# Kernel optimization log

Hardware: AMD Instinct MI355X
Metric: run time of the kernel (lower is better)

The kernel has to match this reference:

```python
import jax, jax.numpy as jnp
import numpy as np

NUM_CLASSES = 81
THRESHOLD = 0.5
NEGPOS_RATIO = 3
VAR0, VAR1 = 0.1, 0.2
B, P, T = 64, 25000, 16


def setup_inputs() -> dict:
    key = jax.random.key(0)
    k1, k2, k3, k4, k5, k6 = jax.random.split(key, 6)
    loc_data = jax.random.normal(k1, (B, P, 4), dtype=jnp.float32)
    conf_data = jax.random.normal(k2, (B, P, NUM_CLASSES), dtype=jnp.float32)
    # priors in center-offset form (cx, cy, w, h), all in (0,1), w/h > 0
    centers = jax.random.uniform(k3, (P, 2), minval=0.05, maxval=0.95)
    wh = jax.random.uniform(k4, (P, 2), minval=0.05, maxval=0.3)
    priors = jnp.concatenate([centers, wh], axis=1).astype(jnp.float32)
    # ground-truth boxes in corner form (xmin, ymin, xmax, ymax), valid (max > min)
    pts = jax.random.uniform(k5, (B, T, 2, 2), minval=0.0, maxval=0.98)
    mn = jnp.min(pts, axis=2)
    mx = jnp.max(pts, axis=2) + 0.02  # strictly positive width/height
    boxes = jnp.concatenate([mn, jnp.clip(mx, 0.0, 1.0)], axis=-1)
    labels = jax.random.randint(k6, (B, T), 0, NUM_CLASSES - 1).astype(jnp.float32)
    targets = jnp.concatenate([boxes, labels[..., None]], axis=-1)
    return {"loc_data": loc_data, "conf_data": conf_data, "priors": priors, "targets": targets}


def point_form(p):
    # (cx,cy,w,h) -> (xmin,ymin,xmax,ymax)
    return jnp.concatenate([p[:, :2] - p[:, 2:] / 2, p[:, :2] + p[:, 2:] / 2], axis=1)


def jaccard(a, b):
    # a: [T,4], b: [P,4], corner form -> IoU [T,P]
    lt = jnp.maximum(a[:, None, :2], b[None, :, :2])
    rb = jnp.minimum(a[:, None, 2:], b[None, :, 2:])
    wh = jnp.clip(rb - lt, 0.0)
    inter = wh[..., 0] * wh[..., 1]
    area_a = ((a[:, 2] - a[:, 0]) * (a[:, 3] - a[:, 1]))[:, None]
    area_b = ((b[:, 2] - b[:, 0]) * (b[:, 3] - b[:, 1]))[None, :]
    return inter / (area_a + area_b - inter)


def encode(matched, priors):
    # SSD offset encoding with variances
    g_cxcy = ((matched[:, :2] + matched[:, 2:]) * 0.5 - priors[:, :2]) / (VAR0 * priors[:, 2:])
    g_wh = jnp.log((matched[:, 2:] - matched[:, :2]) / priors[:, 2:]) / VAR1
    return jnp.concatenate([g_cxcy, g_wh], axis=1)


def match_one(truths, labels, priors):
    # truths: [T,4] corner, labels: [T], priors: [P,4] center
    overlaps = jaccard(truths, point_form(priors))        # [T,P]
    best_prior_idx = jnp.argmax(overlaps, axis=1)         # [T]
    best_truth_overlap = jnp.max(overlaps, axis=0)        # [P]
    best_truth_idx = jnp.argmax(overlaps, axis=0)         # [P]
    best_truth_overlap = best_truth_overlap.at[best_prior_idx].set(2.0)
    for j in range(T):
        best_truth_idx = best_truth_idx.at[best_prior_idx[j]].set(j)
    matched = truths[best_truth_idx]                      # [P,4]
    conf = labels[best_truth_idx].astype(jnp.int32) + 1
    conf = jnp.where(best_truth_overlap < THRESHOLD, 0, conf)
    return encode(matched, priors), conf


def smooth_l1(d):
    ad = jnp.abs(d)
    return jnp.where(ad < 1.0, 0.5 * d * d, ad - 0.5)


def reference(loc_data, conf_data, priors, targets):
    truths = jax.lax.stop_gradient(targets[..., :4])  # .data in torch
    labels = jax.lax.stop_gradient(targets[..., 4])
    loc_t, conf_t = jax.vmap(match_one, in_axes=(0, 0, None))(truths, labels, priors)
    pos = conf_t > 0                                      # [B,P]
    num_priors = pos.shape[1]
    # localization: smooth-L1 summed over positive priors (masked instead of boolean gather)
    loss_l = jnp.sum(jnp.where(pos[..., None], smooth_l1(loc_data - loc_t), 0.0))
    # per-prior conf loss = logsumexp - logit[target]
    lse = jax.nn.logsumexp(conf_data, axis=-1)            # [B,P]
    conf_gt = jnp.take_along_axis(conf_data, conf_t[..., None], axis=-1)[..., 0]
    ce = lse - conf_gt
    # hard negative mining: zero positives, double argsort rank
    loss_c = jnp.where(pos, 0.0, ce)
    loss_idx = jnp.argsort(-loss_c, axis=1)
    idx_rank = jnp.argsort(loss_idx, axis=1)
    num_pos = jnp.sum(pos, axis=1, keepdims=True)
    num_neg = jnp.minimum(NEGPOS_RATIO * num_pos, num_priors - 1)
    neg = idx_rank < num_neg
    # cross-entropy summed over positives + mined negatives
    loss_conf = jnp.sum(jnp.where(pos | neg, ce, 0.0))
    N = jnp.maximum(jnp.sum(num_pos).astype(loc_data.dtype), 1.0)
    return loss_l / N, loss_conf / N
```

## Files before the change

### kernel.cpp

```cpp
#include <hip/hip_runtime.h>

namespace {

constexpr int kB = 64;
constexpr int kP = 25000;
constexpr int kT = 16;
constexpr int kC = 81;
constexpr int kRowsPerBlk = 64;
constexpr int kChunks = 16;
constexpr int kChunkP = (kP + kChunks - 1) / kChunks;
constexpr float kThresh = 0.5f;

__device__ __forceinline__ float smooth_l1(float d) {
  float ad = fabsf(d);
  return ad < 1.0f ? 0.5f * d * d : ad - 0.5f;
}

__global__ __launch_bounds__(256) void match1_kernel(
    const float* __restrict__ priors,
    const float* __restrict__ targets,
    unsigned char* __restrict__ mcode,
    unsigned long long* __restrict__ best_prior) {
  const int chunk = blockIdx.x;
  const int b = blockIdx.y;
  const int tid = threadIdx.x;
  const int p0 = chunk * kChunkP;
  const int p1 = min(p0 + kChunkP, kP);

  __shared__ float tx0[kT], ty0[kT], tx1[kT], ty1[kT], tarea[kT];
  __shared__ float swv[kT][4];
  __shared__ int swi[kT][4];

  if (tid < kT) {
    const float* tg = targets + (b * kT + tid) * 5;
    float x0 = tg[0], y0 = tg[1], x1 = tg[2], y1 = tg[3];
    tx0[tid] = x0; ty0[tid] = y0; tx1[tid] = x1; ty1[tid] = y1;
    tarea[tid] = (x1 - x0) * (y1 - y0);
  }
  __syncthreads();

  float bestv[kT];
  int besti[kT];
#pragma unroll
  for (int t = 0; t < kT; ++t) { bestv[t] = -1.0f; besti[t] = 0; }

  for (int p = p0 + tid; p < p1; p += 256) {
    float4 pr = reinterpret_cast<const float4*>(priors)[p];
    float px0 = pr.x - pr.z * 0.5f, py0 = pr.y - pr.w * 0.5f;
    float px1 = pr.x + pr.z * 0.5f, py1 = pr.y + pr.w * 0.5f;
    float parea = (px1 - px0) * (py1 - py0);
    float mv = -1.0f;
    int mt = 0;
#pragma unroll
    for (int t = 0; t < kT; ++t) {
      float lx = fmaxf(tx0[t], px0), ly = fmaxf(ty0[t], py0);
      float rx = fminf(tx1[t], px1), ry = fminf(ty1[t], py1);
      float w = fmaxf(rx - lx, 0.0f), h = fmaxf(ry - ly, 0.0f);
      float inter = w * h;
      float iou = inter / (tarea[t] + parea - inter);
      if (iou > bestv[t]) { bestv[t] = iou; besti[t] = p; }
      if (iou > mv) { mv = iou; mt = t; }
    }
    mcode[b * kP + p] = (unsigned char)(mt | (mv < kThresh ? 0x80 : 0));
  }

#pragma unroll
  for (int t = 0; t < kT; ++t) {
    float v = bestv[t];
    int i = besti[t];
    for (int off = 32; off > 0; off >>= 1) {
      float v2 = __shfl_xor(v, off, 64);
      int i2 = __shfl_xor(i, off, 64);
      if (v2 > v || (v2 == v && i2 < i)) { v = v2; i = i2; }
    }
    if ((tid & 63) == 0) { swv[t][tid >> 6] = v; swi[t][tid >> 6] = i; }
  }
  __syncthreads();
  if (tid < kT) {
    float v = swv[tid][0];
    int i = swi[tid][0];
#pragma unroll
    for (int w = 1; w < 4; ++w) {
      float v2 = swv[tid][w];
      int i2 = swi[tid][w];
      if (v2 > v || (v2 == v && i2 < i)) { v = v2; i = i2; }
    }
    unsigned long long pk = ((unsigned long long)__float_as_uint(v) << 32) |
                            (unsigned long long)(0xFFFFFFFFu - (unsigned)i);
    atomicMax(&best_prior[b * kT + tid], pk);
  }
}

__global__ __launch_bounds__(256) void match2_kernel(
    const float* __restrict__ loc_data,
    const float* __restrict__ priors,
    const float* __restrict__ targets,
    const unsigned long long* __restrict__ best_prior,
    unsigned char* __restrict__ code,
    int* __restrict__ num_pos,
    float* __restrict__ loss_l_acc) {
  const int chunk = blockIdx.x;
  const int b = blockIdx.y;
  const int tid = threadIdx.x;
  const int p0 = chunk * kChunkP;
  const int p1 = min(p0 + kChunkP, kP);

  __shared__ int s_bp[kT];
  __shared__ float sx0[kT], sy0[kT], sx1[kT], sy1[kT], slab[kT];
  __shared__ float swf[4];
  __shared__ int swi[4];

  if (tid < kT) {
    s_bp[tid] = (int)(0xFFFFFFFFu -
                      (unsigned)(best_prior[b * kT + tid] & 0xFFFFFFFFull));
    const float* tg = targets + (b * kT + tid) * 5;
    sx0[tid] = tg[0]; sy0[tid] = tg[1]; sx1[tid] = tg[2]; sy1[tid] = tg[3];
    slab[tid] = tg[4];
  }
  __syncthreads();

  float lsum = 0.0f;
  int pcount = 0;
  for (int p = p0 + tid; p < p1; p += 256) {
    int c = code[b * kP + p];
    int mt = c & 0x0F;
    bool neg = (c & 0x80) != 0;
    bool forced = false;
#pragma unroll
    for (int j = 0; j < kT; ++j) {
      if (s_bp[j] == p) { mt = j; forced = true; }
    }
    int conf = (!forced && neg) ? 0 : ((int)slab[mt] + 1);
    code[b * kP + p] = (unsigned char)conf;
    if (conf > 0) {
      ++pcount;
      float4 pr = reinterpret_cast<const float4*>(priors)[p];
      float mx0 = sx0[mt], my0 = sy0[mt], mx1 = sx1[mt], my1 = sy1[mt];
      float gcx = ((mx0 + mx1) * 0.5f - pr.x) / (0.1f * pr.z);
      float gcy = ((my0 + my1) * 0.5f - pr.y) / (0.1f * pr.w);
      float gw = logf((mx1 - mx0) / pr.z) / 0.2f;
      float gh = logf((my1 - my0) / pr.w) / 0.2f;
      float4 ld = reinterpret_cast<const float4*>(loc_data)[b * kP + p];
      lsum += smooth_l1(ld.x - gcx) + smooth_l1(ld.y - gcy) +
              smooth_l1(ld.z - gw) + smooth_l1(ld.w - gh);
    }
  }
  for (int off = 32; off > 0; off >>= 1) {
    lsum += __shfl_down(lsum, off, 64);
    pcount += __shfl_down(pcount, off, 64);
  }
  if ((tid & 63) == 0) { swf[tid >> 6] = lsum; swi[tid >> 6] = pcount; }
  __syncthreads();
  if (tid == 0) {
    float lt = swf[0] + swf[1] + swf[2] + swf[3];
    int pt = swi[0] + swi[1] + swi[2] + swi[3];
    if (lt != 0.0f) atomicAdd(loss_l_acc, lt);
    if (pt != 0) atomicAdd(&num_pos[b], pt);
  }
}

__global__ __launch_bounds__(256) void ce_kernel(
    const float* __restrict__ conf_data,
    const unsigned char* __restrict__ conf_t,
    float* __restrict__ loss_c,
    float* __restrict__ pos_ce_acc) {
  __shared__ float tile[kRowsPerBlk * kC];
  __shared__ float swsum[4];
  const int tid = threadIdx.x;
  const long long base = (long long)blockIdx.x * (kRowsPerBlk * kC);
  const float4* src = reinterpret_cast<const float4*>(conf_data + base);
  float4* dst = reinterpret_cast<float4*>(tile);
#pragma unroll
  for (int i = 0; i < 6; ++i) {
    int idx = tid + i * 256;
    if (idx < kRowsPerBlk * kC / 4) dst[idx] = src[idx];
  }
  __syncthreads();

  const int r = tid >> 2;
  const int sub = tid & 3;
  const float* x = tile + r * kC;
  float m = -3.0e38f;
  for (int j = sub; j < kC; j += 4) m = fmaxf(m, x[j]);
  m = fmaxf(m, __shfl_xor(m, 1, 64));
  m = fmaxf(m, __shfl_xor(m, 2, 64));
  float s = 0.0f;
  for (int j = sub; j < kC; j += 4) s += __expf(x[j] - m);
  s += __shfl_xor(s, 1, 64);
  s += __shfl_xor(s, 2, 64);
  float posce = 0.0f;
  if (sub == 0) {
    const long long row = (long long)blockIdx.x * kRowsPerBlk + r;
    float lse = __logf(s) + m;
    int ct = conf_t[row];
    float ce = lse - x[ct];
    bool pos = ct > 0;
    loss_c[row] = pos ? 0.0f : ce;
    posce = pos ? ce : 0.0f;
  }
  for (int off = 32; off > 0; off >>= 1) posce += __shfl_down(posce, off, 64);
  if ((tid & 63) == 0) swsum[tid >> 6] = posce;
  __syncthreads();
  if (tid == 0) {
    float t = swsum[0] + swsum[1] + swsum[2] + swsum[3];
    if (t != 0.0f) atomicAdd(pos_ce_acc, t);
  }
}

__global__ __launch_bounds__(256) void select_kernel(
    const float* __restrict__ loss_c,
    const int* __restrict__ num_pos,
    float* __restrict__ acc,
    int* __restrict__ counter,
    float* __restrict__ out) {
  const int b = blockIdx.x;
  const int tid = threadIdx.x;
  const int k = min(3 * num_pos[b], kP - 1);
  __shared__ int swi[4];
  __shared__ float swf[4];

  if (k > 0) {
    constexpr int kV4 = kP / 4;
    constexpr int kPer = (kV4 + 255) / 256;
    const float4* v4 = reinterpret_cast<const float4*>(loss_c + (long long)b * kP);
    float4 lv[kPer];
#pragma unroll
    for (int j = 0; j < kPer; ++j) {
      int i = tid + j * 256;
      lv[j] = (i < kV4) ? v4[i] : float4{0.0f, 0.0f, 0.0f, 0.0f};
    }

    unsigned int ans = 0;
    for (int bit = 30; bit >= 0; --bit) {
      const unsigned int cand = ans | (1u << bit);
      int cnt = 0;
#pragma unroll
      for (int j = 0; j < kPer; ++j) {
        cnt += (__float_as_uint(lv[j].x) >= cand) + (__float_as_uint(lv[j].y) >= cand) +
               (__float_as_uint(lv[j].z) >= cand) + (__float_as_uint(lv[j].w) >= cand);
      }
      for (int off = 32; off > 0; off >>= 1) cnt += __shfl_down(cnt, off, 64);
      if ((tid & 63) == 0) swi[tid >> 6] = cnt;
      __syncthreads();
      int tot = swi[0] + swi[1] + swi[2] + swi[3];
      if (tot >= k) ans = cand;
      __syncthreads();
    }
    float sum = 0.0f;
    int cgt = 0;
#pragma unroll
    for (int j = 0; j < kPer; ++j) {
      if (__float_as_uint(lv[j].x) > ans) { sum += lv[j].x; ++cgt; }
      if (__float_as_uint(lv[j].y) > ans) { sum += lv[j].y; ++cgt; }
      if (__float_as_uint(lv[j].z) > ans) { sum += lv[j].z; ++cgt; }
      if (__float_as_uint(lv[j].w) > ans) { sum += lv[j].w; ++cgt; }
    }
    for (int off = 32; off > 0; off >>= 1) {
      sum += __shfl_down(sum, off, 64);
      cgt += __shfl_down(cgt, off, 64);
    }
    if ((tid & 63) == 0) { swf[tid >> 6] = sum; swi[tid >> 6] = cgt; }
    __syncthreads();
    if (tid == 0) {
      float st = swf[0] + swf[1] + swf[2] + swf[3];
      int ct = swi[0] + swi[1] + swi[2] + swi[3];
      atomicAdd(acc + 2, st + (float)(k - ct) * __uint_as_float(ans));
    }
  }

  __threadfence();
  if (tid == 0) {
    int done = atomicAdd(counter, 1);
    if (done == kB - 1) {
      int np = 0;
      for (int i = 0; i < kB; ++i) np += num_pos[i];
      float N = fmaxf((float)np, 1.0f);
      float neg = atomicAdd(acc + 2, 0.0f);
      out[0] = acc[0] / N;
      out[1] = (acc[1] + neg) / N;
    }
  }
}

}

extern "C" void kernel_launch(void* const* d_in, const int* in_sizes, int n_in,
                              void* d_out, int out_size, void* d_ws, size_t ws_size,
                              hipStream_t stream) {
  const float* loc_data = (const float*)d_in[0];
  const float* conf_data = (const float*)d_in[1];
  const float* priors = (const float*)d_in[2];
  const float* targets = (const float*)d_in[3];
  float* out = (float*)d_out;

  char* ws = (char*)d_ws;
  float* loss_c = (float*)ws;
  unsigned char* code = (unsigned char*)(ws + 6400000);
  unsigned long long* best_prior = (unsigned long long*)(ws + 8000000);
  int* num_pos = (int*)(ws + 8008192);
  float* acc = (float*)(ws + 8008448);
  int* counter = (int*)(ws + 8008512);

  hipMemsetAsync(ws + 8000000, 0, 8576, stream);
  hipLaunchKernelGGL(match1_kernel, dim3(kChunks, kB), dim3(256), 0, stream,
                     priors, targets, code, best_prior);
  hipLaunchKernelGGL(match2_kernel, dim3(kChunks, kB), dim3(256), 0, stream,
                     loc_data, priors, targets, best_prior, code, num_pos, acc + 0);
  hipLaunchKernelGGL(ce_kernel, dim3(kB * kP / kRowsPerBlk), dim3(256), 0, stream,
                     conf_data, code, loss_c, acc + 1);
  hipLaunchKernelGGL(select_kernel, dim3(kB), dim3(256), 0, stream,
                     loss_c, num_pos, acc, counter, out);
}
```

Before: 830.3 us.

## Fuse match finalization and localization loss into the cross-entropy kernel

The second matching pass (forced-match resolution, conf target, smooth-L1 localization loss) moves into the per-row cross-entropy kernel, so the code array is no longer rewritten and re-read between kernels. The global atomicMax over best priors becomes per-chunk partial results that the fused kernel reduces on load. The separate memset is dropped by zeroing the accumulators inside the first kernel. This removes one kernel launch, a memset and one pass over the code array, in exchange for redundant best-prior reductions in every CE block and boundary handling for blocks that span two batch items.

```diff
diff --git a/kernel.cpp b/kernel.cpp
--- a/kernel.cpp
+++ b/kernel.cpp
@@ -20,12 +20,21 @@
     const float* __restrict__ priors,
     const float* __restrict__ targets,
     unsigned char* __restrict__ mcode,
-    unsigned long long* __restrict__ best_prior) {
+    unsigned long long* __restrict__ best_pc,
+    int* __restrict__ num_pos,
+    float* __restrict__ acc,
+    int* __restrict__ counter) {
   const int chunk = blockIdx.x;
   const int b = blockIdx.y;
   const int tid = threadIdx.x;
   const int p0 = chunk * kChunkP;
   const int p1 = min(p0 + kChunkP, kP);
+
+  if (chunk == 0 && b == 0) {
+    if (tid < kB) num_pos[tid] = 0;
+    else if (tid < kB + 3) acc[tid - kB] = 0.0f;
+    else if (tid == kB + 3) *counter = 0;
+  }
 
   __shared__ float tx0[kT], ty0[kT], tx1[kT], ty1[kT], tarea[kT];
   __shared__ float swv[kT][4];
@@ -87,93 +96,56 @@
     }
     unsigned long long pk = ((unsigned long long)__float_as_uint(v) << 32) |
                             (unsigned long long)(0xFFFFFFFFu - (unsigned)i);
-    atomicMax(&best_prior[b * kT + tid], pk);
-  }
-}
-
-__global__ __launch_bounds__(256) void match2_kernel(
+    best_pc[((size_t)b * kT + tid) * kChunks + chunk] = pk;
+  }
+}
+
+__global__ __launch_bounds__(256) void ce_fused_kernel(
+    const float* __restrict__ conf_data,
+    const unsigned char* __restrict__ mcode,
     const float* __restrict__ loc_data,
     const float* __restrict__ priors,
     const float* __restrict__ targets,
-    const unsigned long long* __restrict__ best_prior,
-    unsigned char* __restrict__ code,
+    const unsigned long long* __restrict__ best_pc,
+    float* __restrict__ loss_c,
     int* __restrict__ num_pos,
-    float* __restrict__ loss_l_acc) {
-  const int chunk = blockIdx.x;
-  const int b = blockIdx.y;
+    float* __restrict__ acc) {
+  __shared__ float tile[kRowsPerBlk * kC];
+  __shared__ unsigned char smc[kRowsPerBlk];
+  __shared__ int s_bp[2][kT];
+  __shared__ float sx0[2][kT], sy0[2][kT], sx1[2][kT], sy1[2][kT], slab[2][kT];
+  __shared__ float swf_l[4], swf_p[4];
+  __shared__ int swi0[4], swi1[4];
+
   const int tid = threadIdx.x;
-  const int p0 = chunk * kChunkP;
-  const int p1 = min(p0 + kChunkP, kP);
-
-  __shared__ int s_bp[kT];
-  __shared__ float sx0[kT], sy0[kT], sx1[kT], sy1[kT], slab[kT];
-  __shared__ float swf[4];
-  __shared__ int swi[4];
-
-  if (tid < kT) {
-    s_bp[tid] = (int)(0xFFFFFFFFu -
-                      (unsigned)(best_prior[b * kT + tid] & 0xFFFFFFFFull));
-    const float* tg = targets + (b * kT + tid) * 5;
-    sx0[tid] = tg[0]; sy0[tid] = tg[1]; sx1[tid] = tg[2]; sy1[tid] = tg[3];
-    slab[tid] = tg[4];
-  }
-  __syncthreads();
-
-  float lsum = 0.0f;
-  int pcount = 0;
-  for (int p = p0 + tid; p < p1; p += 256) {
-    int c = code[b * kP + p];
-    int mt = c & 0x0F;
-    bool neg = (c & 0x80) != 0;
-    bool forced = false;
-#pragma unroll
-    for (int j = 0; j < kT; ++j) {
-      if (s_bp[j] == p) { mt = j; forced = true; }
-    }
-    int conf = (!forced && neg) ? 0 : ((int)slab[mt] + 1);
-    code[b * kP + p] = (unsigned char)conf;
-    if (conf > 0) {
-      ++pcount;
-      float4 pr = reinterpret_cast<const float4*>(priors)[p];
-      float mx0 = sx0[mt], my0 = sy0[mt], mx1 = sx1[mt], my1 = sy1[mt];
-      float gcx = ((mx0 + mx1) * 0.5f - pr.x) / (0.1f * pr.z);
-      float gcy = ((my0 + my1) * 0.5f - pr.y) / (0.1f * pr.w);
-      float gw = logf((mx1 - mx0) / pr.z) / 0.2f;
-      float gh = logf((my1 - my0) / pr.w) / 0.2f;
-      float4 ld = reinterpret_cast<const float4*>(loc_data)[b * kP + p];
-      lsum += smooth_l1(ld.x - gcx) + smooth_l1(ld.y - gcy) +
-              smooth_l1(ld.z - gw) + smooth_l1(ld.w - gh);
-    }
-  }
-  for (int off = 32; off > 0; off >>= 1) {
-    lsum += __shfl_down(lsum, off, 64);
-    pcount += __shfl_down(pcount, off, 64);
-  }
-  if ((tid & 63) == 0) { swf[tid >> 6] = lsum; swi[tid >> 6] = pcount; }
-  __syncthreads();
-  if (tid == 0) {
-    float lt = swf[0] + swf[1] + swf[2] + swf[3];
-    int pt = swi[0] + swi[1] + swi[2] + swi[3];
-    if (lt != 0.0f) atomicAdd(loss_l_acc, lt);
-    if (pt != 0) atomicAdd(&num_pos[b], pt);
-  }
-}
-
-__global__ __launch_bounds__(256) void ce_kernel(
-    const float* __restrict__ conf_data,
-    const unsigned char* __restrict__ conf_t,
-    float* __restrict__ loss_c,
-    float* __restrict__ pos_ce_acc) {
-  __shared__ float tile[kRowsPerBlk * kC];
-  __shared__ float swsum[4];
-  const int tid = threadIdx.x;
-  const long long base = (long long)blockIdx.x * (kRowsPerBlk * kC);
-  const float4* src = reinterpret_cast<const float4*>(conf_data + base);
+  const long long base = (long long)blockIdx.x * kRowsPerBlk;
+  const int b0 = (int)(base / kP);
+  const long long split = (long long)(b0 + 1) * kP;
+
+  const float4* src = reinterpret_cast<const float4*>(conf_data + base * kC);
   float4* dst = reinterpret_cast<float4*>(tile);
 #pragma unroll
   for (int i = 0; i < 6; ++i) {
     int idx = tid + i * 256;
     if (idx < kRowsPerBlk * kC / 4) dst[idx] = src[idx];
+  }
+  if (tid < kRowsPerBlk / 4)
+    reinterpret_cast<unsigned int*>(smc)[tid] =
+        reinterpret_cast<const unsigned int*>(mcode + base)[tid];
+  if (tid < 2 * kT) {
+    const int which = tid >> 4, t = tid & 15;
+    const int b = b0 + which;
+    if (b < kB) {
+      const unsigned long long* pc = best_pc + ((size_t)b * kT + t) * kChunks;
+      unsigned long long m = pc[0];
+#pragma unroll
+      for (int c = 1; c < kChunks; ++c) { unsigned long long v = pc[c]; m = v > m ? v : m; }
+      s_bp[which][t] = (int)(0xFFFFFFFFu - (unsigned)(m & 0xFFFFFFFFull));
+      const float* tg = targets + ((size_t)b * kT + t) * 5;
+      sx0[which][t] = tg[0]; sy0[which][t] = tg[1];
+      sx1[which][t] = tg[2]; sy1[which][t] = tg[3];
+      slab[which][t] = tg[4];
+    }
   }
   __syncthreads();
 
@@ -188,22 +160,61 @@
   for (int j = sub; j < kC; j += 4) s += __expf(x[j] - m);
   s += __shfl_xor(s, 1, 64);
   s += __shfl_xor(s, 2, 64);
-  float posce = 0.0f;
+
+  float lsum = 0.0f, posce = 0.0f;
+  int pc0 = 0, pc1 = 0;
   if (sub == 0) {
-    const long long row = (long long)blockIdx.x * kRowsPerBlk + r;
+    const long long row = base + r;
+    const int which = (row >= split) ? 1 : 0;
+    const int p = (int)(row - (long long)(b0 + which) * kP);
+    int c = smc[r];
+    int mt = c & 0x0F;
+    bool neg = (c & 0x80) != 0;
+    bool forced = false;
+#pragma unroll
+    for (int j = 0; j < kT; ++j) {
+      if (s_bp[which][j] == p) { mt = j; forced = true; }
+    }
+    int conf = (!forced && neg) ? 0 : ((int)slab[which][mt] + 1);
     float lse = __logf(s) + m;
-    int ct = conf_t[row];
-    float ce = lse - x[ct];
-    bool pos = ct > 0;
+    float ce = lse - x[conf];
+    bool pos = conf > 0;
     loss_c[row] = pos ? 0.0f : ce;
     posce = pos ? ce : 0.0f;
-  }
-  for (int off = 32; off > 0; off >>= 1) posce += __shfl_down(posce, off, 64);
-  if ((tid & 63) == 0) swsum[tid >> 6] = posce;
+    if (pos) {
+      float4 pr = reinterpret_cast<const float4*>(priors)[p];
+      float mx0 = sx0[which][mt], my0 = sy0[which][mt];
+      float mx1 = sx1[which][mt], my1 = sy1[which][mt];
+      float gcx = ((mx0 + mx1) * 0.5f - pr.x) / (0.1f * pr.z);
+      float gcy = ((my0 + my1) * 0.5f - pr.y) / (0.1f * pr.w);
+      float gw = logf((mx1 - mx0) / pr.z) / 0.2f;
+      float gh = logf((my1 - my0) / pr.w) / 0.2f;
+      float4 ld = reinterpret_cast<const float4*>(loc_data)[row];
+      lsum = smooth_l1(ld.x - gcx) + smooth_l1(ld.y - gcy) +
+             smooth_l1(ld.z - gw) + smooth_l1(ld.w - gh);
+      if (which) pc1 = 1; else pc0 = 1;
+    }
+  }
+  for (int off = 32; off > 0; off >>= 1) {
+    posce += __shfl_down(posce, off, 64);
+    lsum += __shfl_down(lsum, off, 64);
+    pc0 += __shfl_down(pc0, off, 64);
+    pc1 += __shfl_down(pc1, off, 64);
+  }
+  if ((tid & 63) == 0) {
+    swf_p[tid >> 6] = posce; swf_l[tid >> 6] = lsum;
+    swi0[tid >> 6] = pc0;    swi1[tid >> 6] = pc1;
+  }
   __syncthreads();
   if (tid == 0) {
-    float t = swsum[0] + swsum[1] + swsum[2] + swsum[3];
-    if (t != 0.0f) atomicAdd(pos_ce_acc, t);
+    float tp = swf_p[0] + swf_p[1] + swf_p[2] + swf_p[3];
+    float tl = swf_l[0] + swf_l[1] + swf_l[2] + swf_l[3];
+    int t0 = swi0[0] + swi0[1] + swi0[2] + swi0[3];
+    int t1 = swi1[0] + swi1[1] + swi1[2] + swi1[3];
+    if (tl != 0.0f) atomicAdd(acc + 0, tl);
+    if (tp != 0.0f) atomicAdd(acc + 1, tp);
+    if (t0) atomicAdd(&num_pos[b0], t0);
+    if (t1) atomicAdd(&num_pos[b0 + 1], t1);
   }
 }
 
@@ -295,19 +306,17 @@
 
   char* ws = (char*)d_ws;
   float* loss_c = (float*)ws;
-  unsigned char* code = (unsigned char*)(ws + 6400000);
-  unsigned long long* best_prior = (unsigned long long*)(ws + 8000000);
-  int* num_pos = (int*)(ws + 8008192);
-  float* acc = (float*)(ws + 8008448);
-  int* counter = (int*)(ws + 8008512);
-
-  hipMemsetAsync(ws + 8000000, 0, 8576, stream);
+  unsigned char* mcode = (unsigned char*)(ws + 6400000);
+  unsigned long long* best_pc = (unsigned long long*)(ws + 8000000);
+  int* num_pos = (int*)(ws + 8131072);
+  float* acc = (float*)(ws + 8131328);
+  int* counter = (int*)(ws + 8131392);
+
   hipLaunchKernelGGL(match1_kernel, dim3(kChunks, kB), dim3(256), 0, stream,
-                     priors, targets, code, best_prior);
-  hipLaunchKernelGGL(match2_kernel, dim3(kChunks, kB), dim3(256), 0, stream,
-                     loc_data, priors, targets, best_prior, code, num_pos, acc + 0);
-  hipLaunchKernelGGL(ce_kernel, dim3(kB * kP / kRowsPerBlk), dim3(256), 0, stream,
-                     conf_data, code, loss_c, acc + 1);
+                     priors, targets, mcode, best_pc, num_pos, acc, counter);
+  hipLaunchKernelGGL(ce_fused_kernel, dim3(kB * kP / kRowsPerBlk), dim3(256), 0,
+                     stream, conf_data, mcode, loc_data, priors, targets,
+                     best_pc, loss_c, num_pos, acc);
   hipLaunchKernelGGL(select_kernel, dim3(kB), dim3(256), 0, stream,
                      loss_c, num_pos, acc, counter, out);
 }
```

Measured after the change: 985.8 us. 18.7% more time.

## Replace memset and atomicMax with per-chunk best-prior slots; register-cache CE row

Applied to the files above, without the earlier changes.

Removes the hipMemsetAsync by zeroing the accumulators inside match1, and replaces the global atomicMax on best prior with per-chunk partial writes that match2 reduces over 16 slots. The CE kernel now loads each thread's 20 contiguous logits into registers once instead of reading shared memory twice with stride 4. This saves a launch and some atomics, but relies on match1 finishing its zeroing before match2 and later kernels run, and contiguous per-thread shared reads may cause bank conflicts.

```diff
diff --git a/kernel.cpp b/kernel.cpp
--- a/kernel.cpp
+++ b/kernel.cpp
@@ -20,12 +20,21 @@
     const float* __restrict__ priors,
     const float* __restrict__ targets,
     unsigned char* __restrict__ mcode,
-    unsigned long long* __restrict__ best_prior) {
+    unsigned long long* __restrict__ best_pc,
+    int* __restrict__ num_pos,
+    float* __restrict__ acc,
+    int* __restrict__ counter) {
   const int chunk = blockIdx.x;
   const int b = blockIdx.y;
   const int tid = threadIdx.x;
   const int p0 = chunk * kChunkP;
   const int p1 = min(p0 + kChunkP, kP);
+
+  if (chunk == 0 && b == 0) {
+    if (tid < kB) num_pos[tid] = 0;
+    else if (tid < kB + 3) acc[tid - kB] = 0.0f;
+    else if (tid == kB + 3) *counter = 0;
+  }
 
   __shared__ float tx0[kT], ty0[kT], tx1[kT], ty1[kT], tarea[kT];
   __shared__ float swv[kT][4];
@@ -87,7 +96,7 @@
     }
     unsigned long long pk = ((unsigned long long)__float_as_uint(v) << 32) |
                             (unsigned long long)(0xFFFFFFFFu - (unsigned)i);
-    atomicMax(&best_prior[b * kT + tid], pk);
+    best_pc[((size_t)b * kT + tid) * kChunks + chunk] = pk;
   }
 }
 
@@ -95,7 +104,7 @@
     const float* __restrict__ loc_data,
     const float* __restrict__ priors,
     const float* __restrict__ targets,
-    const unsigned long long* __restrict__ best_prior,
+    const unsigned long long* __restrict__ best_pc,
     unsigned char* __restrict__ code,
     int* __restrict__ num_pos,
     float* __restrict__ loss_l_acc) {
@@ -111,8 +120,14 @@
   __shared__ int swi[4];
 
   if (tid < kT) {
-    s_bp[tid] = (int)(0xFFFFFFFFu -
-                      (unsigned)(best_prior[b * kT + tid] & 0xFFFFFFFFull));
+    const unsigned long long* pc = best_pc + ((size_t)b * kT + tid) * kChunks;
+    unsigned long long m = pc[0];
+#pragma unroll
+    for (int c = 1; c < kChunks; ++c) {
+      unsigned long long v = pc[c];
+      m = v > m ? v : m;
+    }
+    s_bp[tid] = (int)(0xFFFFFFFFu - (unsigned)(m & 0xFFFFFFFFull));
     const float* tg = targets + (b * kT + tid) * 5;
     sx0[tid] = tg[0]; sy0[tid] = tg[1]; sx1[tid] = tg[2]; sy1[tid] = tg[3];
     slab[tid] = tg[4];
@@ -180,14 +195,27 @@
   const int r = tid >> 2;
   const int sub = tid & 3;
   const float* x = tile + r * kC;
-  float m = -3.0e38f;
-  for (int j = sub; j < kC; j += 4) m = fmaxf(m, x[j]);
+
+  float xv[20];
+  const float* xs = x + 20 * sub;
+#pragma unroll
+  for (int i = 0; i < 20; ++i) xv[i] = xs[i];
+  float x80 = x[80];
+
+  float m = xv[0];
+#pragma unroll
+  for (int i = 1; i < 20; ++i) m = fmaxf(m, xv[i]);
+  m = fmaxf(m, x80);
   m = fmaxf(m, __shfl_xor(m, 1, 64));
   m = fmaxf(m, __shfl_xor(m, 2, 64));
+
   float s = 0.0f;
-  for (int j = sub; j < kC; j += 4) s += __expf(x[j] - m);
+#pragma unroll
+  for (int i = 0; i < 20; ++i) s += __expf(xv[i] - m);
+  if (sub == 0) s += __expf(x80 - m);
   s += __shfl_xor(s, 1, 64);
   s += __shfl_xor(s, 2, 64);
+
   float posce = 0.0f;
   if (sub == 0) {
     const long long row = (long long)blockIdx.x * kRowsPerBlk + r;
@@ -296,16 +324,15 @@
   char* ws = (char*)d_ws;
   float* loss_c = (float*)ws;
   unsigned char* code = (unsigned char*)(ws + 6400000);
-  unsigned long long* best_prior = (unsigned long long*)(ws + 8000000);
-  int* num_pos = (int*)(ws + 8008192);
-  float* acc = (float*)(ws + 8008448);
-  int* counter = (int*)(ws + 8008512);
-
-  hipMemsetAsync(ws + 8000000, 0, 8576, stream);
+  unsigned long long* best_pc = (unsigned long long*)(ws + 8000000);
+  int* num_pos = (int*)(ws + 8131072);
+  float* acc = (float*)(ws + 8131328);
+  int* counter = (int*)(ws + 8131392);
+
   hipLaunchKernelGGL(match1_kernel, dim3(kChunks, kB), dim3(256), 0, stream,
-                     priors, targets, code, best_prior);
+                     priors, targets, code, best_pc, num_pos, acc, counter);
   hipLaunchKernelGGL(match2_kernel, dim3(kChunks, kB), dim3(256), 0, stream,
-                     loc_data, priors, targets, best_prior, code, num_pos, acc + 0);
+                     loc_data, priors, targets, best_pc, code, num_pos, acc + 0);
   hipLaunchKernelGGL(ce_kernel, dim3(kB * kP / kRowsPerBlk), dim3(256), 0, stream,
                      conf_data, code, loss_c, acc + 1);
   hipLaunchKernelGGL(select_kernel, dim3(kB), dim3(256), 0, stream,
```

After: 827.8 us. About the same (-0.3%).
